# Kernel tuning notes

Measured on AMD Instinct MI355X. Metric: run time of the kernel, lower is better.

Reference implementation:

```python
import jax, jax.numpy as jnp
import numpy as np

INP_SIZE = 1024
D_MODEL = 1024
B, S = 4, 2048


def setup_inputs() -> dict:
    key = jax.random.key(0)
    ks = jax.random.split(key, 9)
    q = jax.random.normal(ks[0], (B, S, INP_SIZE), dtype=jnp.float32)
    k = jax.random.normal(ks[1], (B, S, INP_SIZE), dtype=jnp.float32)
    v = jax.random.normal(ks[2], (B, S, INP_SIZE), dtype=jnp.float32)
    mask = jnp.zeros((1, S, S), dtype=jnp.float32)
    # learned params (random_normal init in keras)
    kernel_q = jax.random.normal(ks[3], (INP_SIZE, D_MODEL), dtype=jnp.float32) * 0.05
    kernel_k = jax.random.normal(ks[4], (INP_SIZE, D_MODEL), dtype=jnp.float32) * 0.05
    kernel_v = jax.random.normal(ks[5], (INP_SIZE, D_MODEL), dtype=jnp.float32) * 0.05
    bias_q = jax.random.normal(ks[6], (D_MODEL,), dtype=jnp.float32) * 0.05
    bias_k = jax.random.normal(ks[7], (D_MODEL,), dtype=jnp.float32) * 0.05
    bias_v = jax.random.normal(ks[8], (D_MODEL,), dtype=jnp.float32) * 0.05
    return {"q": q, "k": k, "v": v, "mask": mask,
            "kernel_q": kernel_q, "bias_q": bias_q,
            "kernel_k": kernel_k, "bias_k": bias_k,
            "kernel_v": kernel_v, "bias_v": bias_v}


def reference(q, k, v, mask, kernel_q, bias_q, kernel_k, bias_k, kernel_v, bias_v):
    # QKV projections (note: the original stores gelu activations but never
    # applies them in call(), so none are applied here).
    qp = jnp.einsum('bsi,id->bsd', q, kernel_q) + bias_q  # [B,S,D]
    kp = jnp.einsum('bsi,id->bsd', k, kernel_k) + bias_k
    vp = jnp.einsum('bsi,id->bsd', v, kernel_v) + bias_v
    dk = jnp.asarray(kp.shape[-1], dtype=jnp.float32)
    logits = jnp.einsum('bqd,bkd->bqk', qp, kp) / jnp.sqrt(dk)  # [B,S,S]
    logits = logits + mask  # additive mask, broadcasts over batch
    attn = jax.nn.softmax(logits, axis=-1)
    out = jnp.einsum('bqk,bkd->bqd', attn, vp)  # [B,S,D]
    return out
```

## Files before the change

kernel.cpp:

```cpp
#include <hip/hip_runtime.h>

typedef unsigned short u16;
typedef unsigned int u32;
typedef float f32x4 __attribute__((ext_vector_type(4)));
typedef __bf16 bf16x8 __attribute__((ext_vector_type(8)));

__device__ __forceinline__ u16 f2bf(float f) {
  u32 u = __float_as_uint(f);
  u += 0x7fffu + ((u >> 16) & 1u);
  return (u16)(u >> 16);
}
__device__ __forceinline__ float bf2f(u16 s) { return __uint_as_float(((u32)s) << 16); }
__device__ __forceinline__ float bf2f_lo(u32 w) { return __uint_as_float(w << 16); }
__device__ __forceinline__ float bf2f_hi(u32 w) { return __uint_as_float(w & 0xffff0000u); }

__device__ __forceinline__ void gload_lds16(const u16* g, u16* l) {
  __builtin_amdgcn_global_load_lds((const __attribute__((address_space(1))) void*)g,
                                   (__attribute__((address_space(3))) void*)l, 16, 0, 0);
}

__global__ __launch_bounds__(256)
void convert3_f32_bf16(const float* __restrict__ a, const float* __restrict__ b,
                       const float* __restrict__ c, u16* __restrict__ dst0, long n) {
  const float* src = blockIdx.z == 0 ? a : (blockIdx.z == 1 ? b : c);
  u16* dst = dst0 + (long)blockIdx.z * n;
  long stride = (long)gridDim.x * blockDim.x * 4;
  for (long i = ((long)blockIdx.x * blockDim.x + threadIdx.x) * 4; i < n; i += stride) {
    float4 v = *(const float4*)(src + i);
    ushort4 o;
    o.x = f2bf(v.x); o.y = f2bf(v.y); o.z = f2bf(v.z); o.w = f2bf(v.w);
    *(ushort4*)(dst + i) = o;
  }
}

__global__ __launch_bounds__(256)
void wtrans(const float* __restrict__ w0, const float* __restrict__ w1,
            const float* __restrict__ w2, u16* __restrict__ out0) {
  const float* src = blockIdx.z == 0 ? w0 : (blockIdx.z == 1 ? w1 : w2);
  u16* dst = out0 + (long)blockIdx.z * 1048576;
  __shared__ float tile[64][65];
  int t = threadIdx.x;
  int r = t >> 4, c4 = (t & 15) * 4;
  int kb = blockIdx.y * 64;
  int nb = blockIdx.x * 64;
#pragma unroll
  for (int rr = 0; rr < 64; rr += 16) {
    float4 v = *(const float4*)(src + (long)(kb + r + rr) * 1024 + nb + c4);
    tile[r + rr][c4 + 0] = v.x;
    tile[r + rr][c4 + 1] = v.y;
    tile[r + rr][c4 + 2] = v.z;
    tile[r + rr][c4 + 3] = v.w;
  }
  __syncthreads();
#pragma unroll
  for (int rr = 0; rr < 64; rr += 16) {
    ushort4 o;
    o.x = f2bf(tile[c4 + 0][r + rr]);
    o.y = f2bf(tile[c4 + 1][r + rr]);
    o.z = f2bf(tile[c4 + 2][r + rr]);
    o.w = f2bf(tile[c4 + 3][r + rr]);
    *(ushort4*)(dst + (long)(nb + r + rr) * 1024 + kb + c4) = o;
  }
}

__global__ __launch_bounds__(256)
void btrans(const u16* __restrict__ in0, u16* __restrict__ out0, int R, int C) {
  const u16* in = in0 + (long)blockIdx.z * R * C;
  u16* out = out0 + (long)blockIdx.z * R * C;
  __shared__ u16 tile[64][66];
  int t = threadIdx.x;
  int r = t >> 4, c4 = (t & 15) * 4;
  long rb = (long)blockIdx.y * 64;
  long cb = (long)blockIdx.x * 64;
#pragma unroll
  for (int rr = 0; rr < 64; rr += 16) {
    ushort4 v = *(const ushort4*)(in + (rb + r + rr) * C + cb + c4);
    tile[r + rr][c4 + 0] = v.x;
    tile[r + rr][c4 + 1] = v.y;
    tile[r + rr][c4 + 2] = v.z;
    tile[r + rr][c4 + 3] = v.w;
  }
  __syncthreads();
#pragma unroll
  for (int rr = 0; rr < 64; rr += 16) {
    ushort4 o;
    o.x = tile[c4 + 0][r + rr];
    o.y = tile[c4 + 1][r + rr];
    o.z = tile[c4 + 2][r + rr];
    o.w = tile[c4 + 3][r + rr];
    *(ushort4*)(out + (cb + r + rr) * R + rb + c4) = o;
  }
}

template <bool OUT_BF16, bool HAS_BIAS>
__global__ __launch_bounds__(256)
void gemm_bt(const u16* __restrict__ A, const u16* __restrict__ B,
             void* __restrict__ C, const float* __restrict__ bias,
             float scale, int M, int N, int K, long sA, long sB, long sC) {
  constexpr int BM = 128, BN = 128, BK = 64;
  __shared__ u16 As[BM * BK];
  __shared__ u16 Bs[BN * BK];
  const int tid = threadIdx.x;
  const int wid = tid >> 6, lane = tid & 63;
  const int wr = wid >> 1, wc = wid & 1;
  const int l15 = lane & 15, l4 = lane >> 4;
  const long z = blockIdx.z;
  const u16* Ab = A + z * sA;
  const u16* Bb = B + z * sB;
  const int bm = blockIdx.x * BM;
  const int bn = blockIdx.y * BN;

  f32x4 acc[4][4] = {};

  const u16* ga[4];
  const u16* gb[4];
  u16* la[4];
  u16* lb[4];
#pragma unroll
  for (int j = 0; j < 4; ++j) {
    int idx = j * 256 + tid;
    int row = idx >> 3, kc = idx & 7;
    ga[j] = Ab + (long)(bm + row) * K + kc * 8;
    gb[j] = Bb + (long)(bn + row) * K + kc * 8;
    la[j] = As + idx * 8;
    lb[j] = Bs + idx * 8;
  }

  for (int kt = 0; kt < K; kt += BK) {
    __syncthreads();
#pragma unroll
    for (int j = 0; j < 4; ++j) {
      gload_lds16(ga[j] + kt, la[j]);
      gload_lds16(gb[j] + kt, lb[j]);
    }
    __syncthreads();
#pragma unroll
    for (int kk = 0; kk < BK; kk += 32) {
      bf16x8 af[4], bfr[4];
#pragma unroll
      for (int i = 0; i < 4; ++i) {
        af[i] = *(const bf16x8*)(As + (wr * 64 + i * 16 + l15) * BK + kk + l4 * 8);
        bfr[i] = *(const bf16x8*)(Bs + (wc * 64 + i * 16 + l15) * BK + kk + l4 * 8);
      }
#pragma unroll
      for (int i = 0; i < 4; ++i)
#pragma unroll
        for (int j = 0; j < 4; ++j)
          acc[i][j] = __builtin_amdgcn_mfma_f32_16x16x32_bf16(af[i], bfr[j], acc[i][j], 0, 0, 0);
    }
  }

#pragma unroll
  for (int j = 0; j < 4; ++j) {
    int col = bn + wc * 64 + j * 16 + l15;
    float bv = HAS_BIAS ? bias[col] : 0.f;
#pragma unroll
    for (int i = 0; i < 4; ++i) {
      int row0 = bm + wr * 64 + i * 16 + l4 * 4;
      f32x4 v = acc[i][j];
#pragma unroll
      for (int r = 0; r < 4; ++r) {
        float x = (v[r] + bv) * scale;
        long off = z * sC + (long)(row0 + r) * N + col;
        if (OUT_BF16)
          ((u16*)C)[off] = f2bf(x);
        else
          ((float*)C)[off] = x;
      }
    }
  }
}

__device__ __forceinline__ float wave_max(float v) {
#pragma unroll
  for (int o = 32; o > 0; o >>= 1) v = fmaxf(v, __shfl_xor(v, o, 64));
  return v;
}
__device__ __forceinline__ float wave_sum(float v) {
#pragma unroll
  for (int o = 32; o > 0; o >>= 1) v += __shfl_xor(v, o, 64);
  return v;
}

__global__ __launch_bounds__(256)
void softmax_mask(u16* __restrict__ S, const float* __restrict__ mask) {
  long row = blockIdx.x;
  int q = (int)(row & 2047);
  u16* sp = S + row * 2048;
  const float* mp = mask + (long)q * 2048;
  int t = threadIdx.x;
  int wid = t >> 6;
  __shared__ float red[8];

  uint4 raw = *(const uint4*)(sp + t * 8);
  float4 m0 = *(const float4*)(mp + t * 8);
  float4 m1 = *(const float4*)(mp + t * 8 + 4);
  float x[8];
  x[0] = bf2f_lo(raw.x) + m0.x;
  x[1] = bf2f_hi(raw.x) + m0.y;
  x[2] = bf2f_lo(raw.y) + m0.z;
  x[3] = bf2f_hi(raw.y) + m0.w;
  x[4] = bf2f_lo(raw.z) + m1.x;
  x[5] = bf2f_hi(raw.z) + m1.y;
  x[6] = bf2f_lo(raw.w) + m1.z;
  x[7] = bf2f_hi(raw.w) + m1.w;

  float mx = x[0];
#pragma unroll
  for (int i = 1; i < 8; ++i) mx = fmaxf(mx, x[i]);
  mx = wave_max(mx);
  if ((t & 63) == 0) red[wid] = mx;
  __syncthreads();
  mx = fmaxf(fmaxf(red[0], red[1]), fmaxf(red[2], red[3]));

  float e[8], s = 0.f;
#pragma unroll
  for (int i = 0; i < 8; ++i) {
    e[i] = __expf(x[i] - mx);
    s += e[i];
  }
  s = wave_sum(s);
  if ((t & 63) == 0) red[4 + wid] = s;
  __syncthreads();
  s = (red[4] + red[5]) + (red[6] + red[7]);
  float inv = 1.f / s;

  uint4 outw;
  outw.x = (u32)f2bf(e[0] * inv) | ((u32)f2bf(e[1] * inv) << 16);
  outw.y = (u32)f2bf(e[2] * inv) | ((u32)f2bf(e[3] * inv) << 16);
  outw.z = (u32)f2bf(e[4] * inv) | ((u32)f2bf(e[5] * inv) << 16);
  outw.w = (u32)f2bf(e[6] * inv) | ((u32)f2bf(e[7] * inv) << 16);
  *(uint4*)(sp + t * 8) = outw;
}

extern "C" void kernel_launch(void* const* d_in, const int* in_sizes, int n_in,
                              void* d_out, int out_size, void* d_ws, size_t ws_size,
                              hipStream_t stream) {
  const float* q = (const float*)d_in[0];
  const float* k = (const float*)d_in[1];
  const float* v = (const float*)d_in[2];
  const float* mask = (const float*)d_in[3];
  const float* wq = (const float*)d_in[4];
  const float* bq = (const float*)d_in[5];
  const float* wk = (const float*)d_in[6];
  const float* bk = (const float*)d_in[7];
  const float* wv = (const float*)d_in[8];
  const float* bv = (const float*)d_in[9];
  float* out = (float*)d_out;

  u16* ws = (u16*)d_ws;
  const long NP = 8388608;
  u16* qp = ws;
  u16* kp = ws + NP;
  u16* vp = ws + 2 * NP;
  u16* wT = ws + 3 * NP;
  u16* conv = ws + 3 * NP + 3145728;
  u16* qb = conv;
  u16* kb = conv + NP;
  u16* vb = conv + 2 * NP;
  u16* S = conv;
  u16* vpT = conv + 2 * NP;

  convert3_f32_bf16<<<dim3(2048, 1, 3), 256, 0, stream>>>(q, k, v, conv, NP);
  wtrans<<<dim3(16, 16, 3), 256, 0, stream>>>(wq, wk, wv, wT);
  gemm_bt<true, true><<<dim3(64, 8, 1), 256, 0, stream>>>(
      qb, wT, (void*)qp, bq, 0.03125f, 8192, 1024, 1024, 0, 0, 0);
  gemm_bt<true, true><<<dim3(64, 8, 1), 256, 0, stream>>>(
      kb, wT + 1048576, (void*)kp, bk, 1.0f, 8192, 1024, 1024, 0, 0, 0);
  gemm_bt<true, true><<<dim3(64, 8, 1), 256, 0, stream>>>(
      vb, wT + 2097152, (void*)vp, bv, 1.0f, 8192, 1024, 1024, 0, 0, 0);
  btrans<<<dim3(16, 32, 4), 256, 0, stream>>>(vp, vpT, 2048, 1024);
  gemm_bt<true, false><<<dim3(16, 16, 4), 256, 0, stream>>>(
      qp, kp, (void*)S, nullptr, 1.0f, 2048, 2048, 1024,
      (long)2048 * 1024, (long)2048 * 1024, (long)2048 * 2048);
  softmax_mask<<<dim3(8192, 1, 1), 256, 0, stream>>>(S, mask);
  gemm_bt<false, false><<<dim3(16, 8, 4), 256, 0, stream>>>(
      S, vpT, (void*)out, nullptr, 1.0f, 2048, 1024, 2048,
      (long)2048 * 2048, (long)1024 * 2048, (long)2048 * 1024);
}
```

Before: 372.0 us.

## Replace GEMMs with 256x256 double-buffered 8-wave pipelined kernel and fuse QKV launches

Replaces the 128x128 single-buffered GEMM with a 256x256-tile, 512-thread kernel. It double-buffers LDS with XOR-swizzled layout, interleaves global-to-LDS staging with MFMA phases using explicit waitcnt, barriers and setprio, and uses a wrap-around prefetch. The three QKV projections become one batched launch, and the V projection epilogue writes transposed output directly, removing the separate transpose kernel. This trades higher register/LDS pressure and fewer, larger blocks, which risks poorer occupancy and tail effects on small grids such as the final 128-block GEMM.

```diff
diff --git a/kernel.cpp b/kernel.cpp
--- a/kernel.cpp
+++ b/kernel.cpp
@@ -10,7 +10,6 @@
   u += 0x7fffu + ((u >> 16) & 1u);
   return (u16)(u >> 16);
 }
-__device__ __forceinline__ float bf2f(u16 s) { return __uint_as_float(((u32)s) << 16); }
 __device__ __forceinline__ float bf2f_lo(u32 w) { return __uint_as_float(w << 16); }
 __device__ __forceinline__ float bf2f_hi(u32 w) { return __uint_as_float(w & 0xffff0000u); }
 
@@ -63,112 +62,179 @@
   }
 }
 
-__global__ __launch_bounds__(256)
-void btrans(const u16* __restrict__ in0, u16* __restrict__ out0, int R, int C) {
-  const u16* in = in0 + (long)blockIdx.z * R * C;
-  u16* out = out0 + (long)blockIdx.z * R * C;
-  __shared__ u16 tile[64][66];
-  int t = threadIdx.x;
-  int r = t >> 4, c4 = (t & 15) * 4;
-  long rb = (long)blockIdx.y * 64;
-  long cb = (long)blockIdx.x * 64;
-#pragma unroll
-  for (int rr = 0; rr < 64; rr += 16) {
-    ushort4 v = *(const ushort4*)(in + (rb + r + rr) * C + cb + c4);
-    tile[r + rr][c4 + 0] = v.x;
-    tile[r + rr][c4 + 1] = v.y;
-    tile[r + rr][c4 + 2] = v.z;
-    tile[r + rr][c4 + 3] = v.w;
-  }
-  __syncthreads();
-#pragma unroll
-  for (int rr = 0; rr < 64; rr += 16) {
-    ushort4 o;
-    o.x = tile[c4 + 0][r + rr];
-    o.y = tile[c4 + 1][r + rr];
-    o.z = tile[c4 + 2][r + rr];
-    o.w = tile[c4 + 3][r + rr];
-    *(ushort4*)(out + (cb + r + rr) * R + rb + c4) = o;
-  }
-}
-
-template <bool OUT_BF16, bool HAS_BIAS>
-__global__ __launch_bounds__(256)
-void gemm_bt(const u16* __restrict__ A, const u16* __restrict__ B,
-             void* __restrict__ C, const float* __restrict__ bias,
-             float scale, int M, int N, int K, long sA, long sB, long sC) {
-  constexpr int BM = 128, BN = 128, BK = 64;
-  __shared__ u16 As[BM * BK];
-  __shared__ u16 Bs[BN * BK];
+template <int MODE>
+__global__ __launch_bounds__(512, 2)
+void gemm8(const u16* __restrict__ A, const u16* __restrict__ B,
+           void* __restrict__ Cn, u16* __restrict__ Cct,
+           const float* __restrict__ bqp, const float* __restrict__ bkp,
+           const float* __restrict__ bvp,
+           int M, int N, int K, long sA, long sB, long sC) {
+  __shared__ u16 lds[2][2][16384];
   const int tid = threadIdx.x;
   const int wid = tid >> 6, lane = tid & 63;
-  const int wr = wid >> 1, wc = wid & 1;
+  const int wr = wid >> 2, wc = wid & 3;
   const int l15 = lane & 15, l4 = lane >> 4;
-  const long z = blockIdx.z;
-  const u16* Ab = A + z * sA;
-  const u16* Bb = B + z * sB;
-  const int bm = blockIdx.x * BM;
-  const int bn = blockIdx.y * BN;
-
-  f32x4 acc[4][4] = {};
-
-  const u16* ga[4];
-  const u16* gb[4];
-  u16* la[4];
-  u16* lb[4];
-#pragma unroll
-  for (int j = 0; j < 4; ++j) {
-    int idx = j * 256 + tid;
-    int row = idx >> 3, kc = idx & 7;
-    ga[j] = Ab + (long)(bm + row) * K + kc * 8;
-    gb[j] = Bb + (long)(bn + row) * K + kc * 8;
-    la[j] = As + idx * 8;
-    lb[j] = Bs + idx * 8;
-  }
-
-  for (int kt = 0; kt < K; kt += BK) {
-    __syncthreads();
-#pragma unroll
-    for (int j = 0; j < 4; ++j) {
-      gload_lds16(ga[j] + kt, la[j]);
-      gload_lds16(gb[j] + kt, lb[j]);
-    }
-    __syncthreads();
-#pragma unroll
-    for (int kk = 0; kk < BK; kk += 32) {
-      bf16x8 af[4], bfr[4];
-#pragma unroll
-      for (int i = 0; i < 4; ++i) {
-        af[i] = *(const bf16x8*)(As + (wr * 64 + i * 16 + l15) * BK + kk + l4 * 8);
-        bfr[i] = *(const bf16x8*)(Bs + (wc * 64 + i * 16 + l15) * BK + kk + l4 * 8);
+  const int z = blockIdx.z;
+  const u16* Ab = A + (long)z * sA;
+  const u16* Bb = B + (long)z * sB;
+  const int bm = blockIdx.x * 256;
+  const int bnn = blockIdx.y * 256;
+
+  f32x4 acc[8][4] = {};
+  bf16x8 af[4][2], pb0[2][2], pb1[2][2];
+
+#define STAGE_A(buf, mh, ks) {                                                \
+    int d_ = ((mh) * 64 * 8) + tid;                                           \
+    int r_ = d_ >> 3; int cs_ = (d_ & 7) ^ (r_ & 7);                          \
+    gload_lds16(Ab + (long)(bm + r_) * K + (ks) + cs_ * 8,                    \
+                &lds[buf][0][d_ * 8]);                                        \
+    d_ += 1024; r_ = d_ >> 3; cs_ = (d_ & 7) ^ (r_ & 7);                      \
+    gload_lds16(Ab + (long)(bm + r_) * K + (ks) + cs_ * 8,                    \
+                &lds[buf][0][d_ * 8]);                                        \
+  }
+
+#define STAGE_B(buf, nh, ks)                                                  \
+  _Pragma("unroll") for (int qq_ = 0; qq_ < 2; ++qq_) {                       \
+    int u_ = qq_ * 512 + tid;                                                 \
+    int s_ = u_ >> 8, w_ = u_ & 255;                                          \
+    int r_ = s_ * 64 + (nh) * 32 + (w_ >> 3);                                 \
+    int cs_ = (w_ & 7) ^ (r_ & 7);                                            \
+    gload_lds16(Bb + (long)(bnn + r_) * K + (ks) + cs_ * 8,                   \
+                &lds[buf][1][(r_ * 8 + (w_ & 7)) * 8]);                       \
+  }
+
+#define LDA(buf, mh)                                                          \
+  _Pragma("unroll") for (int i_ = 0; i_ < 4; ++i_)                            \
+  _Pragma("unroll") for (int kk_ = 0; kk_ < 2; ++kk_) {                       \
+    int r_ = wr * 128 + (mh) * 64 + i_ * 16 + l15;                            \
+    int cb_ = (kk_ * 4 + l4) ^ (r_ & 7);                                      \
+    af[i_][kk_] = *(const bf16x8*)&lds[buf][0][(r_ * 8 + cb_) * 8];           \
+  }
+
+#define LDB(buf, nh, dst)                                                     \
+  _Pragma("unroll") for (int j_ = 0; j_ < 2; ++j_)                            \
+  _Pragma("unroll") for (int kk_ = 0; kk_ < 2; ++kk_) {                       \
+    int r_ = wc * 64 + (nh) * 32 + j_ * 16 + l15;                             \
+    int cb_ = (kk_ * 4 + l4) ^ (r_ & 7);                                      \
+    dst[j_][kk_] = *(const bf16x8*)&lds[buf][1][(r_ * 8 + cb_) * 8];          \
+  }
+
+#define MF(mh, nh, bfr)                                                       \
+  _Pragma("unroll") for (int kk_ = 0; kk_ < 2; ++kk_)                         \
+  _Pragma("unroll") for (int i_ = 0; i_ < 4; ++i_)                            \
+  _Pragma("unroll") for (int j_ = 0; j_ < 2; ++j_)                            \
+    acc[(mh) * 4 + i_][(nh) * 2 + j_] = __builtin_amdgcn_mfma_f32_16x16x32_bf16( \
+        af[i_][kk_], bfr[j_][kk_], acc[(mh) * 4 + i_][(nh) * 2 + j_], 0, 0, 0);
+
+#define BAR __builtin_amdgcn_s_barrier()
+#define LGKM0 asm volatile("s_waitcnt lgkmcnt(0)" ::: "memory")
+#define LGKM8 asm volatile("s_waitcnt lgkmcnt(8)" ::: "memory")
+#define VM6 asm volatile("s_waitcnt vmcnt(6)" ::: "memory")
+#define PRIO1 __builtin_amdgcn_s_setprio(1)
+#define PRIO0 __builtin_amdgcn_s_setprio(0)
+
+  STAGE_A(0, 0, 0); STAGE_B(0, 0, 0); STAGE_B(0, 1, 0); STAGE_A(0, 1, 0);
+  STAGE_A(1, 0, 64); STAGE_B(1, 0, 64); STAGE_B(1, 1, 64);
+  VM6;
+  BAR;
+
+  for (int it = 0, nit = K >> 7; it < nit; ++it) {
+    const int kt1 = it * 128 + 64;
+    int ks0 = it * 128 + 128; if (ks0 >= K) ks0 -= K;
+    int ks1 = kt1 + 128;      if (ks1 >= K) ks1 -= K;
+    LDA(0, 0); LDB(0, 0, pb0); STAGE_A(1, 1, kt1);
+    LGKM8; BAR; LGKM0;
+    PRIO1; MF(0, 0, pb0); PRIO0; BAR;
+    LDB(0, 1, pb1); STAGE_A(0, 0, ks0);
+    BAR; LGKM0;
+    PRIO1; MF(0, 1, pb1); PRIO0; BAR;
+    LDA(0, 1); STAGE_B(0, 0, ks0);
+    BAR; LGKM0;
+    PRIO1; MF(1, 1, pb1); PRIO0; BAR;
+    STAGE_B(0, 1, ks0); VM6;
+    BAR;
+    PRIO1; MF(1, 0, pb0); PRIO0; BAR;
+    LDA(1, 0); LDB(1, 0, pb0); STAGE_A(0, 1, ks0);
+    LGKM8; BAR; LGKM0;
+    PRIO1; MF(0, 0, pb0); PRIO0; BAR;
+    LDB(1, 1, pb1); STAGE_A(1, 0, ks1);
+    BAR; LGKM0;
+    PRIO1; MF(0, 1, pb1); PRIO0; BAR;
+    LDA(1, 1); STAGE_B(1, 0, ks1);
+    BAR; LGKM0;
+    PRIO1; MF(1, 1, pb1); PRIO0; BAR;
+    STAGE_B(1, 1, ks1); VM6;
+    BAR;
+    PRIO1; MF(1, 0, pb0); PRIO0; BAR;
+  }
+  asm volatile("s_waitcnt vmcnt(0)" ::: "memory");
+
+  const int crow0 = bm + wr * 128 + l4 * 4;
+  const int ccol0 = bnn + wc * 64 + l15;
+  if constexpr (MODE == 0) {
+    u16* Cp = (u16*)Cn + (long)z * sC;
+#pragma unroll
+    for (int m = 0; m < 8; ++m)
+#pragma unroll
+      for (int n = 0; n < 4; ++n)
+#pragma unroll
+        for (int r = 0; r < 4; ++r)
+          Cp[(long)(crow0 + m * 16 + r) * N + (ccol0 + n * 16)] = f2bf(acc[m][n][r]);
+  } else if constexpr (MODE == 1) {
+    float* Cp = (float*)Cn + (long)z * sC;
+#pragma unroll
+    for (int m = 0; m < 8; ++m)
+#pragma unroll
+      for (int n = 0; n < 4; ++n)
+#pragma unroll
+        for (int r = 0; r < 4; ++r)
+          Cp[(long)(crow0 + m * 16 + r) * N + (ccol0 + n * 16)] = acc[m][n][r];
+  } else {
+    const float* bias = z == 0 ? bqp : (z == 1 ? bkp : bvp);
+    const float sc = z == 0 ? 0.03125f : 1.0f;
+    if (z < 2) {
+      u16* Cp = (u16*)Cn + (long)z * sC;
+#pragma unroll
+      for (int n = 0; n < 4; ++n) {
+        float bb = bias[ccol0 + n * 16];
+#pragma unroll
+        for (int m = 0; m < 8; ++m)
+#pragma unroll
+          for (int r = 0; r < 4; ++r)
+            Cp[(long)(crow0 + m * 16 + r) * N + (ccol0 + n * 16)] =
+                f2bf((acc[m][n][r] + bb) * sc);
       }
-#pragma unroll
-      for (int i = 0; i < 4; ++i)
-#pragma unroll
-        for (int j = 0; j < 4; ++j)
-          acc[i][j] = __builtin_amdgcn_mfma_f32_16x16x32_bf16(af[i], bfr[j], acc[i][j], 0, 0, 0);
-    }
-  }
-
-#pragma unroll
-  for (int j = 0; j < 4; ++j) {
-    int col = bn + wc * 64 + j * 16 + l15;
-    float bv = HAS_BIAS ? bias[col] : 0.f;
-#pragma unroll
-    for (int i = 0; i < 4; ++i) {
-      int row0 = bm + wr * 64 + i * 16 + l4 * 4;
-      f32x4 v = acc[i][j];
-#pragma unroll
-      for (int r = 0; r < 4; ++r) {
-        float x = (v[r] + bv) * scale;
-        long off = z * sC + (long)(row0 + r) * N + col;
-        if (OUT_BF16)
-          ((u16*)C)[off] = f2bf(x);
-        else
-          ((float*)C)[off] = x;
+    } else {
+      const int batch = bm >> 11;
+      u16* Cp = Cct + (long)batch * 2097152;
+      const int sbase = (bm & 2047) + wr * 128 + l4 * 4;
+#pragma unroll
+      for (int n = 0; n < 4; ++n) {
+        int d = ccol0 + n * 16;
+        float bb = bias[d];
+#pragma unroll
+        for (int m = 0; m < 8; ++m) {
+          ushort4 o;
+          o.x = f2bf(acc[m][n][0] + bb);
+          o.y = f2bf(acc[m][n][1] + bb);
+          o.z = f2bf(acc[m][n][2] + bb);
+          o.w = f2bf(acc[m][n][3] + bb);
+          *(ushort4*)&Cp[(long)d * 2048 + sbase + m * 16] = o;
+        }
       }
     }
   }
+#undef STAGE_A
+#undef STAGE_B
+#undef LDA
+#undef LDB
+#undef MF
+#undef BAR
+#undef LGKM0
+#undef LGKM8
+#undef VM6
+#undef PRIO1
+#undef PRIO0
 }
 
 __device__ __forceinline__ float wave_max(float v) {
@@ -252,29 +318,20 @@
   const long NP = 8388608;
   u16* qp = ws;
   u16* kp = ws + NP;
-  u16* vp = ws + 2 * NP;
+  u16* vpT = ws + 2 * NP;
   u16* wT = ws + 3 * NP;
   u16* conv = ws + 3 * NP + 3145728;
-  u16* qb = conv;
-  u16* kb = conv + NP;
-  u16* vb = conv + 2 * NP;
   u16* S = conv;
-  u16* vpT = conv + 2 * NP;
 
   convert3_f32_bf16<<<dim3(2048, 1, 3), 256, 0, stream>>>(q, k, v, conv, NP);
   wtrans<<<dim3(16, 16, 3), 256, 0, stream>>>(wq, wk, wv, wT);
-  gemm_bt<true, true><<<dim3(64, 8, 1), 256, 0, stream>>>(
-      qb, wT, (void*)qp, bq, 0.03125f, 8192, 1024, 1024, 0, 0, 0);
-  gemm_bt<true, true><<<dim3(64, 8, 1), 256, 0, stream>>>(
-      kb, wT + 1048576, (void*)kp, bk, 1.0f, 8192, 1024, 1024, 0, 0, 0);
-  gemm_bt<true, true><<<dim3(64, 8, 1), 256, 0, stream>>>(
-      vb, wT + 2097152, (void*)vp, bv, 1.0f, 8192, 1024, 1024, 0, 0, 0);
-  btrans<<<dim3(16, 32, 4), 256, 0, stream>>>(vp, vpT, 2048, 1024);
-  gemm_bt<true, false><<<dim3(16, 16, 4), 256, 0, stream>>>(
-      qp, kp, (void*)S, nullptr, 1.0f, 2048, 2048, 1024,
-      (long)2048 * 1024, (long)2048 * 1024, (long)2048 * 2048);
+  gemm8<2><<<dim3(32, 4, 3), 512, 0, stream>>>(
+      conv, wT, (void*)qp, vpT, bq, bk, bv, 8192, 1024, 1024, NP, 1048576, NP);
+  gemm8<0><<<dim3(8, 8, 4), 512, 0, stream>>>(
+      qp, kp, (void*)S, nullptr, nullptr, nullptr, nullptr,
+      2048, 2048, 1024, 2097152, 2097152, 4194304);
   softmax_mask<<<dim3(8192, 1, 1), 256, 0, stream>>>(S, mask);
-  gemm_bt<false, false><<<dim3(16, 8, 4), 256, 0, stream>>>(
-      S, vpT, (void*)out, nullptr, 1.0f, 2048, 1024, 2048,
-      (long)2048 * 2048, (long)1024 * 2048, (long)2048 * 1024);
-}
+  gemm8<1><<<dim3(8, 4, 4), 512, 0, stream>>>(
+      S, vpT, (void*)out, nullptr, nullptr, nullptr, nullptr,
+      2048, 1024, 2048, 4194304, 2097152, 2097152);
+}
```

After: 354.0 us. 1.05x faster.
